# Performance work log

Hardware: AMD Instinct MI355X
Metric: run time of the kernel (lower is better)

The kernel has to match this reference:

```python
import math
import jax, jax.numpy as jnp
import numpy as np

B, S, H = 8, 1024, 1024
NH = 16
HD = H // NH  # 64


def setup_inputs() -> dict:
    key = jax.random.key(0)
    k1, k2, k3, k4 = jax.random.split(key, 4)
    hidden_states = jax.random.normal(k1, (B, S, H), dtype=jnp.float32)
    attention_mask = jax.random.randint(k2, (B, 1, 1, S), 0, 2, dtype=jnp.int32)
    w_qkv = jax.random.normal(k3, (H, 3 * H), dtype=jnp.float32) * (1.0 / math.sqrt(H))
    b_qkv = jax.random.normal(k4, (3 * H,), dtype=jnp.float32) * 0.02
    return {"hidden_states": hidden_states, "attention_mask": attention_mask,
            "w_qkv": w_qkv, "b_qkv": b_qkv}


def reference(hidden_states, attention_mask, w_qkv, b_qkv):
    b, s, _ = hidden_states.shape
    # fused QKV projection: [b, s, 3H]
    qkv = jnp.einsum('bsh,hk->bsk', hidden_states, w_qkv) + b_qkv
    # view (b, s, nh, 3*hd) -> permute -> chunk last dim (per-head q|k|v layout)
    qkv = qkv.reshape(b, s, NH, 3, HD)
    qkv = jnp.transpose(qkv, (0, 2, 1, 3, 4))      # [b, nh, s, 3, hd]
    q, k, v = qkv[..., 0, :], qkv[..., 1, :], qkv[..., 2, :]
    # raw scores, then FusedScaleMaskSoftmax semantics: scale * scores, mask, fp32 softmax
    scores = jnp.einsum('bhqd,bhkd->bhqk', q, k)
    scale = math.sqrt(HD)  # module passes sqrt(head_dim) as multiplicative scale
    scores = scores.astype(jnp.float32) * scale
    mask = attention_mask != 0                     # nonzero -> masked (padding)
    scores = jnp.where(mask, jnp.float32(-10000.0), scores)
    probs = jax.nn.softmax(scores, axis=-1).astype(hidden_states.dtype)
    # dropout prob = 0 -> identity
    context = jnp.einsum('bhqk,bhkd->bhqd', probs, v)
    context = jnp.transpose(context, (0, 2, 1, 3)).reshape(b, s, NH * HD)
    return context
```

## Files before the change

kernel.cpp:

```cpp
#include <hip/hip_runtime.h>
#include <math.h>

#define Bdim 8
#define Sdim 1024
#define Hdim 1024
#define NHd 16
#define HDd 64
#define N3H 3072

#define Q_OFF   0u
#define K_OFF   16777216u
#define V_OFF   33554432u
#define WH_OFF  41943040u
#define WL_OFF  45088768u
#define AHI_OFF 0u
#define ALO_OFF 8388608u

typedef __bf16 bf16x8 __attribute__((ext_vector_type(8)));
typedef float  f32x4  __attribute__((ext_vector_type(4)));

__device__ __forceinline__ unsigned short f2bf(float x) {
  unsigned b = __builtin_bit_cast(unsigned, x);
  return (unsigned short)((b + 0x7FFFu + ((b >> 16) & 1u)) >> 16);
}
__device__ __forceinline__ float bf2f(unsigned short h) {
  unsigned b = ((unsigned)h) << 16;
  return __builtin_bit_cast(float, b);
}
__device__ __forceinline__ void split_hl(float v, unsigned short& h, unsigned short& l) {
  h = f2bf(v);
  l = f2bf(v - bf2f(h));
}
__device__ __forceinline__ void async16(void* lds, const void* g) {
  __builtin_amdgcn_global_load_lds((const __attribute__((address_space(1))) unsigned int*)g,
                                   (__attribute__((address_space(3))) unsigned int*)lds, 16, 0, 0);
}

__global__ __launch_bounds__(256) void convert_AW(
    const float* __restrict__ A, const float* __restrict__ W,
    unsigned short* __restrict__ aout, unsigned short* __restrict__ ws)
{
  __shared__ float T[64][65];
  const int tid = threadIdx.x;
  int bid = blockIdx.x;
  if (bid < 4096) {
    size_t i = ((size_t)bid * 256 + tid) * 8;
    float4 a0 = *(const float4*)&A[i];
    float4 a1 = *(const float4*)&A[i + 4];
    float av[8] = {a0.x, a0.y, a0.z, a0.w, a1.x, a1.y, a1.z, a1.w};
    unsigned short h[8], l[8];
    #pragma unroll
    for (int j = 0; j < 8; ++j) split_hl(av[j], h[j], l[j]);
    *(uint4*)&aout[AHI_OFF + i] = *(uint4*)h;
    *(uint4*)&aout[ALO_OFF + i] = *(uint4*)l;
    return;
  }
  bid -= 4096;
  const int n0 = (bid % (N3H / 64)) * 64;
  const int k0 = (bid / (N3H / 64)) * 64;
  #pragma unroll
  for (int r = 0; r < 4; ++r) {
    int k = r * 16 + (tid >> 4);
    int n = (tid & 15) * 4;
    float4 v = *(const float4*)&W[(size_t)(k0 + k) * N3H + n0 + n];
    T[k][n + 0] = v.x; T[k][n + 1] = v.y; T[k][n + 2] = v.z; T[k][n + 3] = v.w;
  }
  __syncthreads();
  int n = tid >> 2;
  int kl = (tid & 3) * 16;
  unsigned short h[16], l[16];
  #pragma unroll
  for (int i = 0; i < 16; ++i) split_hl(T[kl + i][n], h[i], l[i]);
  size_t base = (size_t)(n0 + n) * 1024 + k0 + kl;
  *(uint4*)&ws[WH_OFF + base]     = *(uint4*)&h[0];
  *(uint4*)&ws[WH_OFF + base + 8] = *(uint4*)&h[8];
  *(uint4*)&ws[WL_OFF + base]     = *(uint4*)&l[0];
  *(uint4*)&ws[WL_OFF + base + 8] = *(uint4*)&l[8];
}

__global__ __launch_bounds__(256, 2) void qkv_mfma(
    const unsigned short* __restrict__ ao,
    const unsigned short* __restrict__ ws,
    const float* __restrict__ bias,
    unsigned short* __restrict__ wso)
{
  __shared__ unsigned short sA[2][128 * 32];
  __shared__ unsigned short sB[2][128 * 32];

  const int tid  = threadIdx.x;
  const int wave = tid >> 6;
  const int lane = tid & 63;
  const int l16  = lane & 15;
  const int quad = lane >> 4;

  const int n0 = blockIdx.x * 128;
  const int m0 = blockIdx.y * 128;
  const int wm = (wave >> 1) * 64;
  const int wn = (wave & 1) * 64;

  const unsigned short* Ah = ao + AHI_OFF;
  const unsigned short* Al = ao + ALO_OFF;
  const unsigned short* Wh = ws + WH_OFF;
  const unsigned short* Wl = ws + WL_OFF;

  f32x4 acc[4][4];
  #pragma unroll
  for (int i = 0; i < 4; ++i)
    #pragma unroll
    for (int j = 0; j < 4; ++j) acc[i][j] = (f32x4){0.f, 0.f, 0.f, 0.f};

  for (int kt = 0; kt < 1024; kt += 32) {
    __syncthreads();
    #pragma unroll
    for (int r = 0; r < 2; ++r) {
      int chunk = r * 256 + tid;
      int row = chunk >> 2;
      int c8  = (chunk & 3) << 3;
      int ldsoff = (r * 256 + wave * 64) * 8;
      async16(&sA[0][ldsoff], &Ah[(size_t)(m0 + row) * 1024 + kt + c8]);
      async16(&sA[1][ldsoff], &Al[(size_t)(m0 + row) * 1024 + kt + c8]);
      async16(&sB[0][ldsoff], &Wh[(size_t)(n0 + row) * 1024 + kt + c8]);
      async16(&sB[1][ldsoff], &Wl[(size_t)(n0 + row) * 1024 + kt + c8]);
    }
    __syncthreads();

    bf16x8 af[4][2], bf[4][2];
    #pragma unroll
    for (int i = 0; i < 4; ++i) {
      int row = wm + i * 16 + l16;
      af[i][0] = *(const bf16x8*)&sA[0][row * 32 + quad * 8];
      af[i][1] = *(const bf16x8*)&sA[1][row * 32 + quad * 8];
    }
    #pragma unroll
    for (int j = 0; j < 4; ++j) {
      int row = wn + j * 16 + l16;
      bf[j][0] = *(const bf16x8*)&sB[0][row * 32 + quad * 8];
      bf[j][1] = *(const bf16x8*)&sB[1][row * 32 + quad * 8];
    }
    #pragma unroll
    for (int i = 0; i < 4; ++i)
      #pragma unroll
      for (int j = 0; j < 4; ++j) {
        acc[i][j] = __builtin_amdgcn_mfma_f32_16x16x32_bf16(af[i][0], bf[j][0], acc[i][j], 0, 0, 0);
        acc[i][j] = __builtin_amdgcn_mfma_f32_16x16x32_bf16(af[i][1], bf[j][0], acc[i][j], 0, 0, 0);
        acc[i][j] = __builtin_amdgcn_mfma_f32_16x16x32_bf16(af[i][0], bf[j][1], acc[i][j], 0, 0, 0);
      }
  }

  const int ncol0 = n0 + wn;
  const int which = (ncol0 >> 6) % 3;
  const int head  = ncol0 / 192;
  const int mrow0 = m0 + wm;
  const int bb = mrow0 >> 10;
  const int sb = mrow0 & 1023;
  const int bh = bb * NHd + head;

  float bs[4];
  #pragma unroll
  for (int j = 0; j < 4; ++j) bs[j] = bias[ncol0 + j * 16 + l16];

  if (which == 0) {
    unsigned short* dst = wso + Q_OFF + ((size_t)bh * Sdim + sb) * 128;
    #pragma unroll
    for (int i = 0; i < 4; ++i)
      #pragma unroll
      for (int j = 0; j < 4; ++j) {
        int d = j * 16 + l16;
        #pragma unroll
        for (int r = 0; r < 4; ++r) {
          int s = i * 16 + quad * 4 + r;
          unsigned short h, l;
          split_hl(acc[i][j][r] + bs[j], h, l);
          dst[(size_t)s * 128 + d]      = h;
          dst[(size_t)s * 128 + 64 + d] = l;
        }
      }
  } else if (which == 1) {
    unsigned short* dst = wso + K_OFF + (size_t)bh * 131072 + (size_t)(sb >> 6) * 8192;
    #pragma unroll
    for (int i = 0; i < 4; ++i)
      #pragma unroll
      for (int j = 0; j < 4; ++j) {
        int c = j * 16 + l16;
        #pragma unroll
        for (int r = 0; r < 4; ++r) {
          int sp = i * 16 + quad * 4 + r;
          int idx = ((((sp >> 4) * 4 + (c >> 5)) * 64 + ((c >> 3) & 3) * 16 + (sp & 15)) << 3) + (c & 7);
          unsigned short h, l;
          split_hl(acc[i][j][r] + bs[j], h, l);
          dst[idx]        = h;
          dst[idx + 1024] = l;
        }
      }
  } else {
    unsigned short* dst = wso + V_OFF + (size_t)bh * 65536 + (size_t)(sb >> 6) * 4096;
    #pragma unroll
    for (int i = 0; i < 4; ++i)
      #pragma unroll
      for (int j = 0; j < 4; ++j) {
        int dr = j * 16 + l16;
        int ky = i * 16 + quad * 4;
        int idx = ((((dr >> 4) * 2 + (ky >> 5)) * 64 + ((ky >> 3) & 3) * 16 + (dr & 15)) << 3) + (ky & 7);
        unsigned short p[4];
        #pragma unroll
        for (int r = 0; r < 4; ++r) p[r] = f2bf(acc[i][j][r] + bs[j]);
        *(uint2*)&dst[idx] = *(uint2*)p;
      }
  }
}

__global__ __launch_bounds__(256, 3) void attn_mfma(
    const unsigned short* __restrict__ qhl,
    const unsigned short* __restrict__ khl,
    const unsigned short* __restrict__ vt,
    const int* __restrict__ mask,
    float* __restrict__ out)
{
  __shared__ unsigned short Ks[8192];
  __shared__ unsigned short Vs[4096];
  __shared__ unsigned short Pw[4][2048];
  __shared__ float msks[1024];

  const int tid  = threadIdx.x;
  const int wave = tid >> 6;
  const int lane = tid & 63;
  const int l16  = lane & 15;
  const int quad = lane >> 4;

  const int xcd = blockIdx.x & 7;
  const int s_  = blockIdx.x >> 3;
  const int bh  = xcd + ((s_ & 7) << 3) + ((s_ >> 6) << 6);
  const int qt  = (s_ >> 3) & 7;
  const int bb  = bh >> 4;
  const int q0  = qt * 128;

  const unsigned short* kplane = khl + (size_t)bh * 131072;
  const unsigned short* vplane = vt  + (size_t)bh * 65536;

  {
    int4 mv = *(const int4*)&mask[bb * Sdim + tid * 4];
    msks[tid * 4 + 0] = mv.x ? 1.f : 0.f;
    msks[tid * 4 + 1] = mv.y ? 1.f : 0.f;
    msks[tid * 4 + 2] = mv.z ? 1.f : 0.f;
    msks[tid * 4 + 3] = mv.w ? 1.f : 0.f;
  }

  bf16x8 qfA[4], qfB[4];
  {
    int rowA = q0 + wave * 32 + l16;
    const unsigned short* srcA = qhl + ((size_t)bh * Sdim + rowA) * 128;
    const unsigned short* srcB = srcA + 16 * 128;
    #pragma unroll
    for (int kk = 0; kk < 4; ++kk) {
      qfA[kk] = *(const bf16x8*)&srcA[kk * 32 + quad * 8];
      qfB[kk] = *(const bf16x8*)&srcB[kk * 32 + quad * 8];
    }
  }

  f32x4 OA[4] = {{0.f,0.f,0.f,0.f},{0.f,0.f,0.f,0.f},{0.f,0.f,0.f,0.f},{0.f,0.f,0.f,0.f}};
  f32x4 OB[4] = {{0.f,0.f,0.f,0.f},{0.f,0.f,0.f,0.f},{0.f,0.f,0.f,0.f},{0.f,0.f,0.f,0.f}};
  float mrowA[4] = {-INFINITY,-INFINITY,-INFINITY,-INFINITY};
  float mrowB[4] = {-INFINITY,-INFINITY,-INFINITY,-INFINITY};
  float lrowA[4] = {0.f,0.f,0.f,0.f};
  float lrowB[4] = {0.f,0.f,0.f,0.f};

  #pragma unroll 1
  for (int kt = 0; kt < 16; ++kt) {
    __syncthreads();
    {
      const unsigned short* ksrc = kplane + (size_t)kt * 8192;
      const unsigned short* vsrc = vplane + (size_t)kt * 4096;
      #pragma unroll
      for (int r = 0; r < 4; ++r)
        async16(&Ks[(r * 256 + tid) * 8], &ksrc[(size_t)(r * 256 + tid) * 8]);
      #pragma unroll
      for (int r = 0; r < 2; ++r)
        async16(&Vs[(r * 256 + tid) * 8], &vsrc[(size_t)(r * 256 + tid) * 8]);
    }
    __syncthreads();

    f32x4 scA[4], scB[4];
    __builtin_amdgcn_s_setprio(1);
    #pragma unroll
    for (int ns = 0; ns < 4; ++ns) {
      bf16x8 kf0 = *(const bf16x8*)&Ks[((ns * 4 + 0) * 64 + lane) * 8];
      bf16x8 kf1 = *(const bf16x8*)&Ks[((ns * 4 + 1) * 64 + lane) * 8];
      bf16x8 kf2 = *(const bf16x8*)&Ks[((ns * 4 + 2) * 64 + lane) * 8];
      bf16x8 kf3 = *(const bf16x8*)&Ks[((ns * 4 + 3) * 64 + lane) * 8];
      f32x4 cA = {0.f,0.f,0.f,0.f}, cB = {0.f,0.f,0.f,0.f};
      cA = __builtin_amdgcn_mfma_f32_16x16x32_bf16(qfA[0], kf0, cA, 0, 0, 0);
      cB = __builtin_amdgcn_mfma_f32_16x16x32_bf16(qfB[0], kf0, cB, 0, 0, 0);
      cA = __builtin_amdgcn_mfma_f32_16x16x32_bf16(qfA[1], kf1, cA, 0, 0, 0);
      cB = __builtin_amdgcn_mfma_f32_16x16x32_bf16(qfB[1], kf1, cB, 0, 0, 0);
      cA = __builtin_amdgcn_mfma_f32_16x16x32_bf16(qfA[2], kf0, cA, 0, 0, 0);
      cB = __builtin_amdgcn_mfma_f32_16x16x32_bf16(qfB[2], kf0, cB, 0, 0, 0);
      cA = __builtin_amdgcn_mfma_f32_16x16x32_bf16(qfA[3], kf1, cA, 0, 0, 0);
      cB = __builtin_amdgcn_mfma_f32_16x16x32_bf16(qfB[3], kf1, cB, 0, 0, 0);
      cA = __builtin_amdgcn_mfma_f32_16x16x32_bf16(qfA[0], kf2, cA, 0, 0, 0);
      cB = __builtin_amdgcn_mfma_f32_16x16x32_bf16(qfB[0], kf2, cB, 0, 0, 0);
      cA = __builtin_amdgcn_mfma_f32_16x16x32_bf16(qfA[1], kf3, cA, 0, 0, 0);
      cB = __builtin_amdgcn_mfma_f32_16x16x32_bf16(qfB[1], kf3, cB, 0, 0, 0);
      scA[ns] = cA; scB[ns] = cB;
    }
    __builtin_amdgcn_s_setprio(0);

    float rmaxA[4] = {-INFINITY,-INFINITY,-INFINITY,-INFINITY};
    float rmaxB[4] = {-INFINITY,-INFINITY,-INFINITY,-INFINITY};
    #pragma unroll
    for (int ns = 0; ns < 4; ++ns) {
      float mk = msks[kt * 64 + ns * 16 + l16];
      #pragma unroll
      for (int r = 0; r < 4; ++r) {
        float sA2 = (mk != 0.f) ? -10000.f : scA[ns][r] * 8.f;
        float sB2 = (mk != 0.f) ? -10000.f : scB[ns][r] * 8.f;
        scA[ns][r] = sA2; scB[ns][r] = sB2;
        rmaxA[r] = fmaxf(rmaxA[r], sA2);
        rmaxB[r] = fmaxf(rmaxB[r], sB2);
      }
    }
    #pragma unroll
    for (int r = 0; r < 4; ++r) {
      float vA = rmaxA[r], vB = rmaxB[r];
      vA = fmaxf(vA, __shfl_xor(vA, 1, 16)); vB = fmaxf(vB, __shfl_xor(vB, 1, 16));
      vA = fmaxf(vA, __shfl_xor(vA, 2, 16)); vB = fmaxf(vB, __shfl_xor(vB, 2, 16));
      vA = fmaxf(vA, __shfl_xor(vA, 4, 16)); vB = fmaxf(vB, __shfl_xor(vB, 4, 16));
      vA = fmaxf(vA, __shfl_xor(vA, 8, 16)); vB = fmaxf(vB, __shfl_xor(vB, 8, 16));
      rmaxA[r] = vA; rmaxB[r] = vB;
    }

    bool nosk = !(rmaxA[0] <= mrowA[0] + 8.f && rmaxA[1] <= mrowA[1] + 8.f &&
                  rmaxA[2] <= mrowA[2] + 8.f && rmaxA[3] <= mrowA[3] + 8.f &&
                  rmaxB[0] <= mrowB[0] + 8.f && rmaxB[1] <= mrowB[1] + 8.f &&
                  rmaxB[2] <= mrowB[2] + 8.f && rmaxB[3] <= mrowB[3] + 8.f);
    if (__any((int)nosk)) {
      #pragma unroll
      for (int r = 0; r < 4; ++r) {
        float mnA = fmaxf(mrowA[r], rmaxA[r]);
        float mnB = fmaxf(mrowB[r], rmaxB[r]);
        float aA = __expf(mrowA[r] - mnA);
        float aB = __expf(mrowB[r] - mnB);
        mrowA[r] = mnA; mrowB[r] = mnB;
        lrowA[r] *= aA;  lrowB[r] *= aB;
        #pragma unroll
        for (int d = 0; d < 4; ++d) { OA[d][r] *= aA; OB[d][r] *= aB; }
      }
    }

    float rsumA[4] = {0.f,0.f,0.f,0.f}, rsumB[4] = {0.f,0.f,0.f,0.f};
    #pragma unroll
    for (int ns = 0; ns < 4; ++ns) {
      int key = ns * 16 + l16;
      int cbase = (((key >> 5) * 4 + ((key >> 3) & 3)) * 16 + quad * 4) * 8 + (key & 7);
      #pragma unroll
      for (int r = 0; r < 4; ++r) {
        float pA = __expf(scA[ns][r] - mrowA[r]);
        float pB = __expf(scB[ns][r] - mrowB[r]);
        rsumA[r] += pA; rsumB[r] += pB;
        Pw[wave][cbase + r * 8]        = f2bf(pA);
        Pw[wave][1024 + cbase + r * 8] = f2bf(pB);
      }
    }
    #pragma unroll
    for (int r = 0; r < 4; ++r) {
      float vA = rsumA[r], vB = rsumB[r];
      vA += __shfl_xor(vA, 1, 16); vB += __shfl_xor(vB, 1, 16);
      vA += __shfl_xor(vA, 2, 16); vB += __shfl_xor(vB, 2, 16);
      vA += __shfl_xor(vA, 4, 16); vB += __shfl_xor(vB, 4, 16);
      vA += __shfl_xor(vA, 8, 16); vB += __shfl_xor(vB, 8, 16);
      lrowA[r] += vA; lrowB[r] += vB;
    }

    bf16x8 pfA[2], pfB[2];
    #pragma unroll
    for (int kk = 0; kk < 2; ++kk) {
      pfA[kk] = *(const bf16x8*)&Pw[wave][((kk * 4 + quad) * 16 + l16) * 8];
      pfB[kk] = *(const bf16x8*)&Pw[wave][1024 + ((kk * 4 + quad) * 16 + l16) * 8];
    }
    __builtin_amdgcn_s_setprio(1);
    #pragma unroll
    for (int d = 0; d < 4; ++d)
      #pragma unroll
      for (int kk = 0; kk < 2; ++kk) {
        bf16x8 vf = *(const bf16x8*)&Vs[((d * 2 + kk) * 64 + lane) * 8];
        OA[d] = __builtin_amdgcn_mfma_f32_16x16x32_bf16(pfA[kk], vf, OA[d], 0, 0, 0);
        OB[d] = __builtin_amdgcn_mfma_f32_16x16x32_bf16(pfB[kk], vf, OB[d], 0, 0, 0);
      }
    __builtin_amdgcn_s_setprio(0);
  }

  const int h = bh & 15;
  #pragma unroll
  for (int r = 0; r < 4; ++r) {
    float invA = 1.f / lrowA[r];
    float invB = 1.f / lrowB[r];
    int qA = q0 + wave * 32 + quad * 4 + r;
    float* dstA = out + ((size_t)bb * Sdim + qA) * Hdim + h * HDd;
    float* dstB = dstA + 16 * Hdim;
    #pragma unroll
    for (int d = 0; d < 4; ++d) {
      dstA[d * 16 + l16] = OA[d][r] * invA;
      dstB[d * 16 + l16] = OB[d][r] * invB;
    }
  }
}

extern "C" void kernel_launch(void* const* d_in, const int* in_sizes, int n_in,
                              void* d_out, int out_size, void* d_ws, size_t ws_size,
                              hipStream_t stream) {
  const float* hs   = (const float*)d_in[0];
  const int*   mask = (const int*)d_in[1];
  const float* w    = (const float*)d_in[2];
  const float* bias = (const float*)d_in[3];
  float* out = (float*)d_out;
  unsigned short* ws = (unsigned short*)d_ws;
  unsigned short* ao = (unsigned short*)d_out;

  convert_AW<<<4096 + (N3H / 64) * (1024 / 64), 256, 0, stream>>>(hs, w, ao, ws);

  qkv_mfma<<<dim3(N3H / 128, 8192 / 128), 256, 0, stream>>>(ao, ws, bias, ws);

  attn_mfma<<<Bdim * NHd * (Sdim / 128), 256, 0, stream>>>(
      ws + Q_OFF, ws + K_OFF, ws + V_OFF, mask, out);
}
```

Measured before the change: 367.2 us.

## Double-buffer K/V tiles in attention kernel to overlap loads with compute

The attention kernel now keeps two shared-memory buffers for K and V tiles. It prefetches the next key tile asynchronously while the current one is used for QK^T, softmax and PV, and has one barrier per iteration instead of two. The goal is to hide global-to-LDS load latency behind the MFMA work. In exchange, LDS use per block grows and the launch bound drops from 3 to 2 blocks per CU, so less occupancy is available to hide latency the other way.

```diff
diff --git a/kernel.cpp b/kernel.cpp
--- a/kernel.cpp
+++ b/kernel.cpp
@@ -209,15 +209,15 @@
   }
 }
 
-__global__ __launch_bounds__(256, 3) void attn_mfma(
+__global__ __launch_bounds__(256, 2) void attn_mfma(
     const unsigned short* __restrict__ qhl,
     const unsigned short* __restrict__ khl,
     const unsigned short* __restrict__ vt,
     const int* __restrict__ mask,
     float* __restrict__ out)
 {
-  __shared__ unsigned short Ks[8192];
-  __shared__ unsigned short Vs[4096];
+  __shared__ unsigned short Ks[2][8192];
+  __shared__ unsigned short Vs[2][4096];
   __shared__ unsigned short Pw[4][2048];
   __shared__ float msks[1024];
 
@@ -237,6 +237,19 @@
   const unsigned short* kplane = khl + (size_t)bh * 131072;
   const unsigned short* vplane = vt  + (size_t)bh * 65536;
 
+#define STAGE(t_, b_) do { \
+    const unsigned short* _ks = kplane + (size_t)(t_) * 8192; \
+    const unsigned short* _vs = vplane + (size_t)(t_) * 4096; \
+    _Pragma("unroll") \
+    for (int r = 0; r < 4; ++r) \
+      async16(&Ks[b_][(r * 256 + tid) * 8], &_ks[(size_t)(r * 256 + tid) * 8]); \
+    _Pragma("unroll") \
+    for (int r = 0; r < 2; ++r) \
+      async16(&Vs[b_][(r * 256 + tid) * 8], &_vs[(size_t)(r * 256 + tid) * 8]); \
+  } while (0)
+
+  STAGE(0, 0);
+
   {
     int4 mv = *(const int4*)&mask[bb * Sdim + tid * 4];
     msks[tid * 4 + 0] = mv.x ? 1.f : 0.f;
@@ -257,6 +270,8 @@
     }
   }
 
+  __syncthreads();
+
   f32x4 OA[4] = {{0.f,0.f,0.f,0.f},{0.f,0.f,0.f,0.f},{0.f,0.f,0.f,0.f},{0.f,0.f,0.f,0.f}};
   f32x4 OB[4] = {{0.f,0.f,0.f,0.f},{0.f,0.f,0.f,0.f},{0.f,0.f,0.f,0.f},{0.f,0.f,0.f,0.f}};
   float mrowA[4] = {-INFINITY,-INFINITY,-INFINITY,-INFINITY};
@@ -264,29 +279,20 @@
   float lrowA[4] = {0.f,0.f,0.f,0.f};
   float lrowB[4] = {0.f,0.f,0.f,0.f};
 
+  int cur = 0;
+
   #pragma unroll 1
   for (int kt = 0; kt < 16; ++kt) {
-    __syncthreads();
-    {
-      const unsigned short* ksrc = kplane + (size_t)kt * 8192;
-      const unsigned short* vsrc = vplane + (size_t)kt * 4096;
-      #pragma unroll
-      for (int r = 0; r < 4; ++r)
-        async16(&Ks[(r * 256 + tid) * 8], &ksrc[(size_t)(r * 256 + tid) * 8]);
-      #pragma unroll
-      for (int r = 0; r < 2; ++r)
-        async16(&Vs[(r * 256 + tid) * 8], &vsrc[(size_t)(r * 256 + tid) * 8]);
-    }
-    __syncthreads();
+    if (kt < 15) STAGE(kt + 1, cur ^ 1);
 
     f32x4 scA[4], scB[4];
     __builtin_amdgcn_s_setprio(1);
     #pragma unroll
     for (int ns = 0; ns < 4; ++ns) {
-      bf16x8 kf0 = *(const bf16x8*)&Ks[((ns * 4 + 0) * 64 + lane) * 8];
-      bf16x8 kf1 = *(const bf16x8*)&Ks[((ns * 4 + 1) * 64 + lane) * 8];
-      bf16x8 kf2 = *(const bf16x8*)&Ks[((ns * 4 + 2) * 64 + lane) * 8];
-      bf16x8 kf3 = *(const bf16x8*)&Ks[((ns * 4 + 3) * 64 + lane) * 8];
+      bf16x8 kf0 = *(const bf16x8*)&Ks[cur][((ns * 4 + 0) * 64 + lane) * 8];
+      bf16x8 kf1 = *(const bf16x8*)&Ks[cur][((ns * 4 + 1) * 64 + lane) * 8];
+      bf16x8 kf2 = *(const bf16x8*)&Ks[cur][((ns * 4 + 2) * 64 + lane) * 8];
+      bf16x8 kf3 = *(const bf16x8*)&Ks[cur][((ns * 4 + 3) * 64 + lane) * 8];
       f32x4 cA = {0.f,0.f,0.f,0.f}, cB = {0.f,0.f,0.f,0.f};
       cA = __builtin_amdgcn_mfma_f32_16x16x32_bf16(qfA[0], kf0, cA, 0, 0, 0);
       cB = __builtin_amdgcn_mfma_f32_16x16x32_bf16(qfB[0], kf0, cB, 0, 0, 0);
@@ -381,11 +387,14 @@
     for (int d = 0; d < 4; ++d)
       #pragma unroll
       for (int kk = 0; kk < 2; ++kk) {
-        bf16x8 vf = *(const bf16x8*)&Vs[((d * 2 + kk) * 64 + lane) * 8];
+        bf16x8 vf = *(const bf16x8*)&Vs[cur][((d * 2 + kk) * 64 + lane) * 8];
         OA[d] = __builtin_amdgcn_mfma_f32_16x16x32_bf16(pfA[kk], vf, OA[d], 0, 0, 0);
         OB[d] = __builtin_amdgcn_mfma_f32_16x16x32_bf16(pfB[kk], vf, OB[d], 0, 0, 0);
       }
     __builtin_amdgcn_s_setprio(0);
+
+    __syncthreads();
+    cur ^= 1;
   }
 
   const int h = bh & 15;
@@ -402,6 +411,8 @@
       dstB[d * 16 + l16] = OB[d][r] * invB;
     }
   }
+
+#undef STAGE
 }
 
 extern "C" void kernel_launch(void* const* d_in, const int* in_sizes, int n_in,
```

Result: slower. 380.6 us (+3.7%).
